# Optimization experiments

Hardware: AMD Instinct MI355X
Metric: run time of the kernel (lower is better)

The kernel has to match this reference:

```python
import jax, jax.numpy as jnp
import numpy as np
import hashlib

# Model hyperparameters (from VictorASIFractalLightModel defaults)
B, L, D = 2, 2048, 1024
VOCAB, TOOL_VOCAB = 65536, 128
STEPS = 8            # FractalEmbedding steps -> 2*STEPS = 16 features
N_CONV, N_ATTN = 10, 6
HEADS, Q_GROUPS = 8, 2
HPG = HEADS // Q_GROUPS
HEAD_DIM = D // HEADS
KSIZE = 5
EPS = 1e-5


def _token_to_c(token_ids_np):
    # sha256-based complex constant per token id (exactly as in FractalEmbedding)
    flat = token_ids_np.reshape(-1)
    out = np.empty((flat.size, 2), dtype=np.float32)
    for i, tid in enumerate(flat):
        h = hashlib.sha256(str(int(tid)).encode()).hexdigest()
        out[i, 0] = (int(h[:16], 16) / 2**64 - 0.5) * 2.0
        out[i, 1] = (int(h[16:32], 16) / 2**64 - 0.5) * 2.0
    return out.reshape(token_ids_np.shape + (2,))


def _julia_feats(cs):
    # Vectorized julia iteration, z starts at 0.  cs: [B, L, 2] -> feats [B, L, 2*STEPS]
    cr, ci = cs[..., 0], cs[..., 1]
    zr = jnp.zeros_like(cr)
    zi = jnp.zeros_like(ci)
    feats = []
    for _ in range(STEPS):
        zr, zi = zr * zr - zi * zi + cr, 2.0 * zr * zi + ci
        feats.append(zr)
        feats.append(zi)
    return jnp.stack(feats, axis=-1)


def _layer_norm(x, s, b):
    mu = jnp.mean(x, axis=-1, keepdims=True)
    var = jnp.mean(jnp.square(x - mu), axis=-1, keepdims=True)
    return (x - mu) * jax.lax.rsqrt(var + EPS) * s + b


def _conv_block(x, dw_w, dw_b, pw_w, pw_b, ln_s, ln_b):
    # x: [B, L, D] -> depthwise conv (k=5, same pad) -> pointwise conv to 2D -> GLU -> residual LN
    xc = jnp.transpose(x, (0, 2, 1))  # [B, D, L]
    y = jax.lax.conv_general_dilated(xc, dw_w, (1,), [(KSIZE // 2, KSIZE // 2)],
                                     dimension_numbers=("NCH", "OIH", "NCH"),
                                     feature_group_count=D) + dw_b[None, :, None]
    y = jax.lax.conv_general_dilated(y, pw_w, (1,), [(0, 0)],
                                     dimension_numbers=("NCH", "OIH", "NCH")) + pw_b[None, :, None]
    y = jnp.transpose(y, (0, 2, 1))  # [B, L, 2D]
    a, gate = jnp.split(y, 2, axis=-1)
    return _layer_norm(x + a * jax.nn.sigmoid(gate), ln_s, ln_b)


def _attention(x, qw, kvw, ow, ln_s, ln_b):
    # Grouped-query attention with an explicit (unfused) score tensor, per the source.
    Bx, Lx, Dx = x.shape
    q = (x @ qw).reshape(Bx, Lx, Q_GROUPS, HPG, HEAD_DIM)
    kv = (x @ kvw).reshape(Bx, Lx, HEADS, 2, HEAD_DIM)
    k = kv[..., 0, :].reshape(Bx, Lx, Q_GROUPS, HPG, HEAD_DIM)
    v = kv[..., 1, :].reshape(Bx, Lx, Q_GROUPS, HPG, HEAD_DIM)
    scale = HEAD_DIM ** -0.5
    scores = jnp.einsum("bqghd,bkghd->bghqk", q, k) * scale  # [B, g, hpg, Lq, Lk]
    attn = jax.nn.softmax(scores, axis=-1)
    out = jnp.einsum("bghqk,bkghd->bqghd", attn, v).reshape(Bx, Lx, Dx)
    return _layer_norm(x + out @ ow, ln_s, ln_b)


def setup_inputs() -> dict:
    key = jax.random.key(0)
    ks = jax.random.split(key, 10)
    token_ids = jax.random.randint(ks[0], (B, L), 0, VOCAB)
    cs = jnp.asarray(_token_to_c(np.asarray(token_ids)))
    return {
        "token_ids": token_ids,
        "cs": cs,
        "proj_w": jax.random.normal(ks[1], (2 * STEPS, D), dtype=jnp.float32) * 0.25,
        "emb_scale": jnp.ones((1,), dtype=jnp.float32),
        "conv_dw_w": jax.random.normal(ks[2], (N_CONV, D, 1, KSIZE), dtype=jnp.float32) * 0.2,
        "conv_dw_b": jnp.zeros((N_CONV, D), dtype=jnp.float32),
        "conv_pw_w": jax.random.normal(ks[3], (N_CONV, 2 * D, D, 1), dtype=jnp.float32) * (D ** -0.5),
        "conv_pw_b": jnp.zeros((N_CONV, 2 * D), dtype=jnp.float32),
        "conv_ln_s": jnp.ones((N_CONV, D), dtype=jnp.float32),
        "conv_ln_b": jnp.zeros((N_CONV, D), dtype=jnp.float32),
        "attn_q_w": jax.random.normal(ks[4], (N_ATTN, D, D), dtype=jnp.float32) * (D ** -0.5),
        "attn_kv_w": jax.random.normal(ks[5], (N_ATTN, D, 2 * D), dtype=jnp.float32) * (D ** -0.5),
        "attn_out_w": jax.random.normal(ks[6], (N_ATTN, D, D), dtype=jnp.float32) * (D ** -0.5),
        "attn_ln_s": jnp.ones((N_ATTN, D), dtype=jnp.float32),
        "attn_ln_b": jnp.zeros((N_ATTN, D), dtype=jnp.float32),
        "lm_w": jax.random.normal(ks[7], (D, VOCAB), dtype=jnp.float32) * (D ** -0.5),
        "tool_w": jax.random.normal(ks[8], (D, TOOL_VOCAB), dtype=jnp.float32) * (D ** -0.5),
        "tool_b": jnp.zeros((TOOL_VOCAB,), dtype=jnp.float32),
    }


def reference(token_ids, cs, proj_w, emb_scale, conv_dw_w, conv_dw_b, conv_pw_w, conv_pw_b,
              conv_ln_s, conv_ln_b, attn_q_w, attn_kv_w, attn_out_w, attn_ln_s, attn_ln_b,
              lm_w, tool_w, tool_b):
    feats = _julia_feats(cs)                 # [B, L, 16]
    h = (feats @ proj_w) * emb_scale         # FractalEmbedding
    for i in range(N_CONV):
        h = _conv_block(h, conv_dw_w[i], conv_dw_b[i], conv_pw_w[i], conv_pw_b[i],
                        conv_ln_s[i], conv_ln_b[i])
    for i in range(N_ATTN):
        h = _attention(h, attn_q_w[i], attn_kv_w[i], attn_out_w[i], attn_ln_s[i], attn_ln_b[i])
    # ReplayMemoryStack is a side-effecting identity on h.
    last = h[:, -1, :]
    gen_logits = last @ lm_w
    tool_logits = last @ tool_w + tool_b
    return gen_logits, tool_logits
```

## Files before the change

kernel.cpp:

```cpp
#include <hip/hip_runtime.h>
#include <hip/hip_bf16.h>
#include <math.h>

#define B_ 2
#define L_ 2048
#define D_ 1024
#define VOCAB_ 65536
#define TOOLV_ 128
#define NCONV_ 10
#define NATTN_ 6
#define HEADS_ 8
#define HD_ 128
#define EPS_ 1e-5f

typedef short bf16x8 __attribute__((ext_vector_type(8)));
typedef short short4v __attribute__((ext_vector_type(4)));
typedef float f32x4 __attribute__((ext_vector_type(4)));
#define MFMA16(a,b,c) __builtin_amdgcn_mfma_f32_16x16x32_bf16(a, b, c, 0, 0, 0)

__device__ inline short f2bf(float f) {
  __hip_bfloat16 h = __float2bfloat16(f);
  return *reinterpret_cast<short*>(&h);
}

__device__ __forceinline__ void gld16(const void* g, void* l) {
  __builtin_amdgcn_global_load_lds(
      (const __attribute__((address_space(1))) unsigned int*)g,
      (__attribute__((address_space(3))) unsigned int*)l, 16, 0, 0);
}

__global__ __launch_bounds__(256) void julia_proj_k(const float* __restrict__ cs,
    const float* __restrict__ pw, const float* __restrict__ esc, float* __restrict__ h) {
  int row = blockIdx.x;
  float cr = cs[2*(size_t)row], ci = cs[2*(size_t)row+1];
  float f[16];
  float zr = 0.f, zi = 0.f;
  #pragma unroll
  for (int s = 0; s < 8; ++s) {
    float nzr = zr*zr - zi*zi + cr;
    float nzi = 2.f*zr*zi + ci;
    zr = nzr; zi = nzi;
    f[2*s] = zr; f[2*s+1] = zi;
  }
  float e = esc[0];
  int d = threadIdx.x * 4;
  float4 acc = {0.f, 0.f, 0.f, 0.f};
  #pragma unroll
  for (int i = 0; i < 16; ++i) {
    float4 pv = *(const float4*)(pw + i*D_ + d);
    acc.x += f[i]*pv.x; acc.y += f[i]*pv.y; acc.z += f[i]*pv.z; acc.w += f[i]*pv.w;
  }
  acc.x *= e; acc.y *= e; acc.z *= e; acc.w *= e;
  *(float4*)(h + (size_t)row*D_ + d) = acc;
}

__global__ __launch_bounds__(256) void dwconv_k(const float* __restrict__ x,
    const float* __restrict__ w, const float* __restrict__ bias, short* __restrict__ y) {
  int idx = blockIdx.x*256 + threadIdx.x;
  int d = (idx & (D_/4 - 1)) * 4;
  int bl = idx >> 8;
  int l = bl & (L_-1);
  size_t bbase = (size_t)(bl >> 11) * L_;
  float4 acc = *(const float4*)(bias + d);
  float wr[4][5];
  #pragma unroll
  for (int j = 0; j < 4; ++j)
    #pragma unroll
    for (int k = 0; k < 5; ++k) wr[j][k] = w[(d+j)*5 + k];
  #pragma unroll
  for (int k = 0; k < 5; ++k) {
    int ll = l + k - 2;
    if (ll >= 0 && ll < L_) {
      float4 xv = *(const float4*)(x + (bbase + ll)*D_ + d);
      acc.x += xv.x*wr[0][k]; acc.y += xv.y*wr[1][k];
      acc.z += xv.z*wr[2][k]; acc.w += xv.w*wr[3][k];
    }
  }
  short4v o = { f2bf(acc.x), f2bf(acc.y), f2bf(acc.z), f2bf(acc.w) };
  ((short4v*)y)[idx] = o;
}

__global__ __launch_bounds__(256) void cvt_bf16_k(const float* __restrict__ x,
    short* __restrict__ y, int n4) {
  int i = blockIdx.x*256 + threadIdx.x;
  if (i >= n4) return;
  float4 v = ((const float4*)x)[i];
  short4v s = { f2bf(v.x), f2bf(v.y), f2bf(v.z), f2bf(v.w) };
  ((short4v*)y)[i] = s;
}

__global__ __launch_bounds__(256) void transp_bf16_k(const float* __restrict__ W0,
    short* __restrict__ WT0, int K, int N, size_t srcStride, size_t dstStride) {
  const float* W = W0 + blockIdx.z*srcStride;
  short* WT = WT0 + blockIdx.z*dstStride;
  __shared__ short t[32][33];
  int n0 = blockIdx.x*32, k0 = blockIdx.y*32;
  int tx = threadIdx.x & 31, ty = threadIdx.x >> 5;
  #pragma unroll
  for (int i = 0; i < 4; ++i) {
    int k = ty + i*8;
    t[tx][k] = f2bf(W[(size_t)(k0+k)*N + n0 + tx]);
  }
  __syncthreads();
  #pragma unroll
  for (int i = 0; i < 4; ++i) {
    int n = ty + i*8;
    WT[(size_t)(n0+n)*K + k0 + tx] = t[n][tx];
  }
}

template<int MODE, bool BIAS>
__global__ __launch_bounds__(256) void gemm_bf16(const short* __restrict__ A,
    const short* __restrict__ Bt, const float* __restrict__ bias,
    float* __restrict__ C, short* __restrict__ obf,
    short* __restrict__ kbf, short* __restrict__ vtbf,
    float scale, int M, int N, int K) {
  __shared__ short As[2*128*32];
  __shared__ short Bs[2*128*32];
  const int tid  = threadIdx.x;
  const int lane = tid & 63;
  const int wave = tid >> 6;
  const int wm = wave >> 1, wn = wave & 1;
  const int g = lane >> 4, c = lane & 15;
  const int m0 = blockIdx.x * 128, n0 = blockIdx.y * 128;

  f32x4 acc[4][4];
  #pragma unroll
  for (int i = 0; i < 4; ++i)
    #pragma unroll
    for (int j = 0; j < 4; ++j) acc[i][j] = (f32x4){0.f,0.f,0.f,0.f};

  const int srow = wave*16 + (lane>>2);
  const int scol = (lane&3)*8;
  const short* aSrc0 = A + (size_t)(m0 + srow)*K + scol;
  const short* aSrc1 = aSrc0 + (size_t)64*K;
  const short* bSrc0 = Bt + (size_t)(n0 + srow)*K + scol;
  const short* bSrc1 = bSrc0 + (size_t)64*K;
  short* AsW = &As[wave*512];
  short* BsW = &Bs[wave*512];

  for (int k0 = 0; k0 < K; k0 += 64) {
    __syncthreads();
    gld16(aSrc0 + k0,      AsW);
    gld16(aSrc1 + k0,      AsW + 2048);
    gld16(aSrc0 + k0 + 32, AsW + 4096);
    gld16(aSrc1 + k0 + 32, AsW + 6144);
    gld16(bSrc0 + k0,      BsW);
    gld16(bSrc1 + k0,      BsW + 2048);
    gld16(bSrc0 + k0 + 32, BsW + 4096);
    gld16(bSrc1 + k0 + 32, BsW + 6144);
    asm volatile("s_waitcnt vmcnt(0)" ::: "memory");
    __syncthreads();

    #pragma unroll
    for (int s = 0; s < 2; ++s) {
      bf16x8 af[4], bfr[4];
      #pragma unroll
      for (int mi = 0; mi < 4; ++mi)
        af[mi] = *(const bf16x8*)&As[s*4096 + (wm*64 + mi*16 + c)*32 + g*8];
      #pragma unroll
      for (int ni = 0; ni < 4; ++ni)
        bfr[ni] = *(const bf16x8*)&Bs[s*4096 + (wn*64 + ni*16 + c)*32 + g*8];
      #pragma unroll
      for (int mi = 0; mi < 4; ++mi)
        #pragma unroll
        for (int ni = 0; ni < 4; ++ni)
          acc[mi][ni] = MFMA16(af[mi], bfr[ni], acc[mi][ni]);
    }
  }

  #pragma unroll
  for (int mi = 0; mi < 4; ++mi) {
    int row = m0 + wm*64 + mi*16 + g*4;
    #pragma unroll
    for (int ni = 0; ni < 4; ++ni) {
      int col = n0 + wn*64 + ni*16 + c;
      if (MODE == 0) {
        float bv = BIAS ? bias[col] : 0.f;
        #pragma unroll
        for (int r = 0; r < 4; ++r)
          C[(size_t)(row+r)*N + col] = acc[mi][ni][r] + bv;
      } else {
        if (col < 1024) {
          #pragma unroll
          for (int r = 0; r < 4; ++r)
            obf[(size_t)(row+r)*1024 + col] = f2bf(acc[mi][ni][r]*scale);
        } else {
          int col2 = col - 1024;
          int hh = col2 >> 8, jj = (col2 >> 7) & 1, d = col2 & 127;
          int bb = row >> 11, l = row & 2047;
          size_t bh = (size_t)bb*8 + hh;
          if (jj == 0) {
            #pragma unroll
            for (int r = 0; r < 4; ++r)
              kbf[(bh*L_ + l + r)*128 + d] = f2bf(acc[mi][ni][r]);
          } else {
            #pragma unroll
            for (int r = 0; r < 4; ++r)
              vtbf[(bh*128 + d)*L_ + l + r] = f2bf(acc[mi][ni][r]);
          }
        }
      }
    }
  }
}

__global__ __launch_bounds__(256) void glu_ln_k(float* __restrict__ h,
    const float* __restrict__ y2, const float* __restrict__ s, const float* __restrict__ b,
    short* __restrict__ bo) {
  int row = blockIdx.x;
  int tid = threadIdx.x;
  int d = tid*4;
  float* xr = h + (size_t)row*D_;
  const float* yr = y2 + (size_t)row*2*D_;
  __shared__ float red[256];
  float4 xv = *(const float4*)(xr + d);
  float4 av = *(const float4*)(yr + d);
  float4 gv = *(const float4*)(yr + D_ + d);
  float v[4];
  v[0] = xv.x + av.x/(1.f + expf(-gv.x));
  v[1] = xv.y + av.y/(1.f + expf(-gv.y));
  v[2] = xv.z + av.z/(1.f + expf(-gv.z));
  v[3] = xv.w + av.w/(1.f + expf(-gv.w));
  red[tid] = v[0]+v[1]+v[2]+v[3]; __syncthreads();
  for (int st = 128; st > 0; st >>= 1) { if (tid < st) red[tid] += red[tid+st]; __syncthreads(); }
  float mu = red[0] * (1.f/D_); __syncthreads();
  float lv = 0.f;
  #pragma unroll
  for (int j = 0; j < 4; ++j) { float dd = v[j]-mu; lv += dd*dd; }
  red[tid] = lv; __syncthreads();
  for (int st = 128; st > 0; st >>= 1) { if (tid < st) red[tid] += red[tid+st]; __syncthreads(); }
  float var = red[0] * (1.f/D_);
  float r = 1.f/sqrtf(var + EPS_);
  float4 sv = *(const float4*)(s + d);
  float4 bv = *(const float4*)(b + d);
  float4 o;
  o.x = (v[0]-mu)*r*sv.x + bv.x;
  o.y = (v[1]-mu)*r*sv.y + bv.y;
  o.z = (v[2]-mu)*r*sv.z + bv.z;
  o.w = (v[3]-mu)*r*sv.w + bv.w;
  *(float4*)(xr + d) = o;
  if (bo) {
    short4v ob = { f2bf(o.x), f2bf(o.y), f2bf(o.z), f2bf(o.w) };
    *(short4v*)(bo + (size_t)row*D_ + d) = ob;
  }
}

__global__ __launch_bounds__(256) void resid_ln_k(float* __restrict__ h,
    const float* __restrict__ proj, const float* __restrict__ s, const float* __restrict__ b,
    short* __restrict__ bo) {
  int row = blockIdx.x;
  int tid = threadIdx.x;
  int d = tid*4;
  float* xr = h + (size_t)row*D_;
  const float* pr = proj + (size_t)row*D_;
  __shared__ float red[256];
  float4 xv = *(const float4*)(xr + d);
  float4 pv = *(const float4*)(pr + d);
  float v[4] = { xv.x+pv.x, xv.y+pv.y, xv.z+pv.z, xv.w+pv.w };
  red[tid] = v[0]+v[1]+v[2]+v[3]; __syncthreads();
  for (int st = 128; st > 0; st >>= 1) { if (tid < st) red[tid] += red[tid+st]; __syncthreads(); }
  float mu = red[0] * (1.f/D_); __syncthreads();
  float lv = 0.f;
  #pragma unroll
  for (int j = 0; j < 4; ++j) { float dd = v[j]-mu; lv += dd*dd; }
  red[tid] = lv; __syncthreads();
  for (int st = 128; st > 0; st >>= 1) { if (tid < st) red[tid] += red[tid+st]; __syncthreads(); }
  float var = red[0] * (1.f/D_);
  float r = 1.f/sqrtf(var + EPS_);
  float4 sv = *(const float4*)(s + d);
  float4 bv = *(const float4*)(b + d);
  float4 o;
  o.x = (v[0]-mu)*r*sv.x + bv.x;
  o.y = (v[1]-mu)*r*sv.y + bv.y;
  o.z = (v[2]-mu)*r*sv.z + bv.z;
  o.w = (v[3]-mu)*r*sv.w + bv.w;
  *(float4*)(xr + d) = o;
  if (bo) {
    short4v ob = { f2bf(o.x), f2bf(o.y), f2bf(o.z), f2bf(o.w) };
    *(short4v*)(bo + (size_t)row*D_ + d) = ob;
  }
}

#define PPITCH 72
__global__ __launch_bounds__(256) void attn2_k(const short* __restrict__ qbf,
    const short* __restrict__ kbf, const short* __restrict__ vtbf,
    short* __restrict__ obf) {
  __shared__ short Ks[64*128];
  __shared__ short Vts[128*64];
  __shared__ short Ps[4*16*PPITCH];

  const int tid  = threadIdx.x;
  const int wave = tid >> 6;
  const int lane = tid & 63;
  const int g    = lane >> 4;
  const int c    = lane & 15;
  const int hh   = blockIdx.y;
  const int b    = blockIdx.z;
  const int q0   = blockIdx.x*64 + wave*16;
  const size_t bh = (size_t)(b*HEADS_ + hh);

  bf16x8 qf[4];
  {
    const short* Qp = qbf + ((size_t)(b*L_ + q0 + c))*D_ + hh*HD_;
    #pragma unroll
    for (int kd = 0; kd < 4; ++kd)
      qf[kd] = *(const bf16x8*)(Qp + kd*32 + g*8);
  }

  f32x4 O[8];
  #pragma unroll
  for (int i = 0; i < 8; ++i) O[i] = (f32x4){0.f,0.f,0.f,0.f};
  float mrun[4] = {-INFINITY,-INFINITY,-INFINITY,-INFINITY};
  float lrun[4] = {0.f,0.f,0.f,0.f};
  short* Pw = Ps + wave*16*PPITCH;

  const short* kBase = kbf + bh*L_*128;
  const short* vBase = vtbf + bh*128*L_;

  for (int t = 0; t < L_/64; ++t) {
    __syncthreads();
    #pragma unroll
    for (int rd = 0; rd < 4; ++rd) {
      int slot = rd*256 + tid;
      int kr = slot >> 4, kj = slot & 15;
      int vr = slot >> 3, vj = slot & 7;
      gld16(kBase + ((size_t)(t*64 + kr))*128 + ((kj ^ (kr & 15)) * 8),
            (char*)Ks + (rd*256 + wave*64)*16);
      gld16(vBase + (size_t)vr*L_ + t*64 + ((vj ^ (vr & 7)) * 8),
            (char*)Vts + (rd*256 + wave*64)*16);
    }
    asm volatile("s_waitcnt vmcnt(0)" ::: "memory");
    __syncthreads();

    f32x4 s[4];
    #pragma unroll
    for (int nc = 0; nc < 4; ++nc) {
      s[nc] = (f32x4){0.f,0.f,0.f,0.f};
      int R = nc*16 + c;
      #pragma unroll
      for (int kd = 0; kd < 4; ++kd) {
        bf16x8 kf = *(const bf16x8*)&Ks[R*128 + (((kd*4 + g) ^ (R & 15)) * 8)];
        s[nc] = MFMA16(qf[kd], kf, s[nc]);
      }
    }

    float tm[4], rsum[4], alpha[4];
    #pragma unroll
    for (int r = 0; r < 4; ++r)
      tm[r] = fmaxf(fmaxf(s[0][r], s[1][r]), fmaxf(s[2][r], s[3][r]));
    #pragma unroll
    for (int r = 0; r < 4; ++r) {
      #pragma unroll
      for (int mask = 1; mask <= 8; mask <<= 1)
        tm[r] = fmaxf(tm[r], __shfl_xor(tm[r], mask));
      float mnew = fmaxf(mrun[r], tm[r]);
      alpha[r] = expf(mrun[r] - mnew);
      mrun[r] = mnew;
      rsum[r] = 0.f;
    }
    #pragma unroll
    for (int nc = 0; nc < 4; ++nc)
      #pragma unroll
      for (int r = 0; r < 4; ++r) {
        float p = expf(s[nc][r] - mrun[r]);
        s[nc][r] = p;
        rsum[r] += p;
      }
    #pragma unroll
    for (int r = 0; r < 4; ++r) {
      #pragma unroll
      for (int mask = 1; mask <= 8; mask <<= 1)
        rsum[r] += __shfl_xor(rsum[r], mask);
      lrun[r] = lrun[r]*alpha[r] + rsum[r];
    }
    #pragma unroll
    for (int nc = 0; nc < 8; ++nc)
      #pragma unroll
      for (int r = 0; r < 4; ++r) O[nc][r] *= alpha[r];

    #pragma unroll
    for (int nc = 0; nc < 4; ++nc)
      #pragma unroll
      for (int r = 0; r < 4; ++r)
        Pw[(g*4+r)*PPITCH + nc*16 + c] = f2bf(s[nc][r]);
    asm volatile("s_waitcnt lgkmcnt(0)" ::: "memory");
    bf16x8 pa0 = *(const bf16x8*)&Pw[c*PPITCH + g*8];
    bf16x8 pa1 = *(const bf16x8*)&Pw[c*PPITCH + 32 + g*8];

    #pragma unroll
    for (int ks = 0; ks < 2; ++ks) {
      #pragma unroll
      for (int nc = 0; nc < 8; ++nc) {
        int R = nc*16 + c;
        bf16x8 vf = *(const bf16x8*)&Vts[R*64 + (((ks*4 + g) ^ (R & 7)) * 8)];
        O[nc] = MFMA16(ks ? pa1 : pa0, vf, O[nc]);
      }
    }
  }

  short* ob = obf + ((size_t)(b*L_ + q0))*D_ + hh*HD_;
  #pragma unroll
  for (int r = 0; r < 4; ++r) {
    float inv = 1.f / lrun[r];
    #pragma unroll
    for (int nc = 0; nc < 8; ++nc)
      ob[(size_t)(g*4+r)*D_ + nc*16 + c] = f2bf(O[nc][r] * inv);
  }
}

__global__ __launch_bounds__(256) void lm_head_part_k(const float* __restrict__ h,
    const float* __restrict__ lm_w, float* __restrict__ part) {
  int tid = threadIdx.x;
  int n = (blockIdx.x*256 + tid)*4;
  int ks = blockIdx.y;
  __shared__ float last0[256], last1[256];
  const float* h0 = h + ((size_t)0*L_ + (L_-1))*D_ + ks*256;
  const float* h1 = h + ((size_t)1*L_ + (L_-1))*D_ + ks*256;
  last0[tid] = h0[tid]; last1[tid] = h1[tid];
  __syncthreads();
  float4 a0 = {0.f,0.f,0.f,0.f}, a1 = {0.f,0.f,0.f,0.f};
  const float* wp = lm_w + (size_t)(ks*256)*VOCAB_ + n;
  for (int kk = 0; kk < 256; ++kk) {
    float4 wv = *(const float4*)(wp + (size_t)kk*VOCAB_);
    float c0 = last0[kk], c1 = last1[kk];
    a0.x += c0*wv.x; a0.y += c0*wv.y; a0.z += c0*wv.z; a0.w += c0*wv.w;
    a1.x += c1*wv.x; a1.y += c1*wv.y; a1.z += c1*wv.z; a1.w += c1*wv.w;
  }
  *(float4*)(part + ((size_t)ks*2 + 0)*VOCAB_ + n) = a0;
  *(float4*)(part + ((size_t)ks*2 + 1)*VOCAB_ + n) = a1;
}

__global__ __launch_bounds__(256) void lm_head_red_k(const float* __restrict__ part,
    float* __restrict__ out) {
  int i = blockIdx.x*256 + threadIdx.x;
  int j = (i*4) / VOCAB_;
  int n = (i*4) & (VOCAB_-1);
  float4 acc = {0.f,0.f,0.f,0.f};
  #pragma unroll
  for (int ks = 0; ks < 4; ++ks) {
    float4 v = *(const float4*)(part + ((size_t)ks*2 + j)*VOCAB_ + n);
    acc.x += v.x; acc.y += v.y; acc.z += v.z; acc.w += v.w;
  }
  *(float4*)(out + (size_t)j*VOCAB_ + n) = acc;
}

__global__ __launch_bounds__(128) void tool_head_k(const float* __restrict__ h,
    const float* __restrict__ tw, const float* __restrict__ tb, float* __restrict__ out) {
  int b = blockIdx.x;
  int tid = threadIdx.x;
  __shared__ float last[D_];
  const float* hr = h + ((size_t)b*L_ + (L_-1))*D_;
  for (int d = tid; d < D_; d += 128) last[d] = hr[d];
  __syncthreads();
  float acc = tb[tid];
  for (int k = 0; k < D_; ++k) acc += last[k]*tw[(size_t)k*TOOLV_ + tid];
  out[(size_t)2*VOCAB_ + (size_t)b*TOOLV_ + tid] = acc;
}

extern "C" void kernel_launch(void* const* d_in, const int* in_sizes, int n_in,
                              void* d_out, int out_size, void* d_ws, size_t ws_size,
                              hipStream_t stream) {
  const float* cs        = (const float*)d_in[1];
  const float* proj_w    = (const float*)d_in[2];
  const float* emb_scale = (const float*)d_in[3];
  const float* conv_dw_w = (const float*)d_in[4];
  const float* conv_dw_b = (const float*)d_in[5];
  const float* conv_pw_w = (const float*)d_in[6];
  const float* conv_pw_b = (const float*)d_in[7];
  const float* conv_ln_s = (const float*)d_in[8];
  const float* conv_ln_b = (const float*)d_in[9];
  const float* attn_q_w  = (const float*)d_in[10];
  const float* attn_kv_w = (const float*)d_in[11];
  const float* attn_out_w= (const float*)d_in[12];
  const float* attn_ln_s = (const float*)d_in[13];
  const float* attn_ln_b = (const float*)d_in[14];
  const float* lm_w      = (const float*)d_in[15];
  const float* tool_w    = (const float*)d_in[16];
  const float* tool_b    = (const float*)d_in[17];

  const int M = B_*L_;
  float* h    = (float*)d_ws;
  float* buf2 = h    + (size_t)M*D_;
  short* kbf  = (short*)(buf2 + (size_t)M*2*D_);
  short* vtbf = kbf + (size_t)B_*HEADS_*L_*128;
  short* abf  = (short*)(vtbf + (size_t)B_*HEADS_*128*L_);
  short* wconv= abf + (size_t)M*D_;
  short* wqkv = wconv + (size_t)NCONV_*2*D_*D_;
  short* wout = wqkv + (size_t)NATTN_*3*D_*D_;
  float* lmpart = (float*)(wout + (size_t)NATTN_*D_*D_);
  short* qbf  = (short*)(buf2 + (size_t)M*D_);

  const float scale = 0.088388347648318447f;

  {
    int n4 = NCONV_*2*D_*D_/4;
    cvt_bf16_k<<<(n4 + 255)/256, 256, 0, stream>>>(conv_pw_w, wconv, n4);
    transp_bf16_k<<<dim3(D_/32, D_/32, NATTN_), 256, 0, stream>>>(
        attn_q_w, wqkv, D_, D_, (size_t)D_*D_, (size_t)3*D_*D_);
    transp_bf16_k<<<dim3((2*D_)/32, D_/32, NATTN_), 256, 0, stream>>>(
        attn_kv_w, wqkv + (size_t)D_*D_, D_, 2*D_, (size_t)D_*2*D_, (size_t)3*D_*D_);
    transp_bf16_k<<<dim3(D_/32, D_/32, NATTN_), 256, 0, stream>>>(
        attn_out_w, wout, D_, D_, (size_t)D_*D_, (size_t)D_*D_);
  }

  julia_proj_k<<<M, 256, 0, stream>>>(cs, proj_w, emb_scale, h);

  for (int i = 0; i < NCONV_; ++i) {
    dwconv_k<<<(M*D_/4)/256, 256, 0, stream>>>(h, conv_dw_w + (size_t)i*D_*5,
                                               conv_dw_b + (size_t)i*D_, abf);
    gemm_bf16<0, true><<<dim3(M/128, (2*D_)/128), 256, 0, stream>>>(
        abf, wconv + (size_t)i*2*D_*D_, conv_pw_b + (size_t)i*2*D_,
        buf2, nullptr, nullptr, nullptr, 1.f, M, 2*D_, D_);
    glu_ln_k<<<M, 256, 0, stream>>>(h, buf2, conv_ln_s + (size_t)i*D_,
                                    conv_ln_b + (size_t)i*D_,
                                    (i == NCONV_-1) ? abf : (short*)nullptr);
  }

  for (int i = 0; i < NATTN_; ++i) {
    gemm_bf16<3, false><<<dim3(M/128, (3*D_)/128), 256, 0, stream>>>(
        abf, wqkv + (size_t)i*3*D_*D_, nullptr, nullptr, qbf, kbf, vtbf,
        scale, M, 3*D_, D_);
    attn2_k<<<dim3(L_/64, HEADS_, B_), 256, 0, stream>>>(qbf, kbf, vtbf, abf);
    gemm_bf16<0, false><<<dim3(M/128, D_/128), 256, 0, stream>>>(
        abf, wout + (size_t)i*D_*D_, nullptr, buf2, nullptr, nullptr, nullptr,
        1.f, M, D_, D_);
    resid_ln_k<<<M, 256, 0, stream>>>(h, buf2, attn_ln_s + (size_t)i*D_,
                                      attn_ln_b + (size_t)i*D_,
                                      (i < NATTN_-1) ? abf : (short*)nullptr);
  }

  lm_head_part_k<<<dim3(VOCAB_/1024, 4), 256, 0, stream>>>(h, lm_w, lmpart);
  lm_head_red_k<<<(2*VOCAB_/4)/256, 256, 0, stream>>>(lmpart, (float*)d_out);
  tool_head_k<<<B_, 128, 0, stream>>>(h, tool_w, tool_b, (float*)d_out);
}
```

Measured before the change: 1.834 ms.

## Double-buffer LDS tiles in GEMM and attention to overlap loads with MFMA

Converts the bf16 GEMM and the flash-attention kernel from a single shared-memory buffer to ping-pong buffers. The next K-tile (or K/V tile) is issued with global_load_lds before the current tile's MFMAs run, with one wait-and-barrier per iteration. The GEMM K step drops from 64 to 32, so it now runs twice as many iterations with one barrier each. Attention LDS use roughly doubles, which may lower occupancy.

```diff
diff --git a/kernel.cpp b/kernel.cpp
--- a/kernel.cpp
+++ b/kernel.cpp
@@ -29,6 +29,12 @@
       (__attribute__((address_space(3))) unsigned int*)l, 16, 0, 0);
 }
 
+__device__ __forceinline__ void sync_prefetch() {
+  asm volatile("s_waitcnt vmcnt(0)" ::: "memory");
+  __builtin_amdgcn_s_barrier();
+  __builtin_amdgcn_sched_barrier(0);
+}
+
 __global__ __launch_bounds__(256) void julia_proj_k(const float* __restrict__ cs,
     const float* __restrict__ pw, const float* __restrict__ esc, float* __restrict__ h) {
   int row = blockIdx.x;
@@ -115,8 +121,8 @@
     float* __restrict__ C, short* __restrict__ obf,
     short* __restrict__ kbf, short* __restrict__ vtbf,
     float scale, int M, int N, int K) {
-  __shared__ short As[2*128*32];
-  __shared__ short Bs[2*128*32];
+  __shared__ short As[2][128*32];
+  __shared__ short Bs[2][128*32];
   const int tid  = threadIdx.x;
   const int lane = tid & 63;
   const int wave = tid >> 6;
@@ -136,36 +142,39 @@
   const short* aSrc1 = aSrc0 + (size_t)64*K;
   const short* bSrc0 = Bt + (size_t)(n0 + srow)*K + scol;
   const short* bSrc1 = bSrc0 + (size_t)64*K;
-  short* AsW = &As[wave*512];
-  short* BsW = &Bs[wave*512];
-
-  for (int k0 = 0; k0 < K; k0 += 64) {
-    __syncthreads();
-    gld16(aSrc0 + k0,      AsW);
-    gld16(aSrc1 + k0,      AsW + 2048);
-    gld16(aSrc0 + k0 + 32, AsW + 4096);
-    gld16(aSrc1 + k0 + 32, AsW + 6144);
-    gld16(bSrc0 + k0,      BsW);
-    gld16(bSrc1 + k0,      BsW + 2048);
-    gld16(bSrc0 + k0 + 32, BsW + 4096);
-    gld16(bSrc1 + k0 + 32, BsW + 6144);
-    asm volatile("s_waitcnt vmcnt(0)" ::: "memory");
-    __syncthreads();
-
-    #pragma unroll
-    for (int s = 0; s < 2; ++s) {
-      bf16x8 af[4], bfr[4];
-      #pragma unroll
-      for (int mi = 0; mi < 4; ++mi)
-        af[mi] = *(const bf16x8*)&As[s*4096 + (wm*64 + mi*16 + c)*32 + g*8];
+  const int woff = wave*512;
+
+  gld16(aSrc0, &As[0][woff]);
+  gld16(aSrc1, &As[0][woff + 2048]);
+  gld16(bSrc0, &Bs[0][woff]);
+  gld16(bSrc1, &Bs[0][woff + 2048]);
+  sync_prefetch();
+
+  const int nt = K >> 5;
+  int cur = 0;
+  for (int t = 0; t < nt; ++t) {
+    if (t + 1 < nt) {
+      int k0 = (t + 1) << 5;
+      gld16(aSrc0 + k0, &As[cur^1][woff]);
+      gld16(aSrc1 + k0, &As[cur^1][woff + 2048]);
+      gld16(bSrc0 + k0, &Bs[cur^1][woff]);
+      gld16(bSrc1 + k0, &Bs[cur^1][woff + 2048]);
+    }
+    bf16x8 af[4], bfr[4];
+    #pragma unroll
+    for (int mi = 0; mi < 4; ++mi)
+      af[mi] = *(const bf16x8*)&As[cur][(wm*64 + mi*16 + c)*32 + g*8];
+    #pragma unroll
+    for (int ni = 0; ni < 4; ++ni)
+      bfr[ni] = *(const bf16x8*)&Bs[cur][(wn*64 + ni*16 + c)*32 + g*8];
+    #pragma unroll
+    for (int mi = 0; mi < 4; ++mi)
       #pragma unroll
       for (int ni = 0; ni < 4; ++ni)
-        bfr[ni] = *(const bf16x8*)&Bs[s*4096 + (wn*64 + ni*16 + c)*32 + g*8];
-      #pragma unroll
-      for (int mi = 0; mi < 4; ++mi)
-        #pragma unroll
-        for (int ni = 0; ni < 4; ++ni)
-          acc[mi][ni] = MFMA16(af[mi], bfr[ni], acc[mi][ni]);
+        acc[mi][ni] = MFMA16(af[mi], bfr[ni], acc[mi][ni]);
+    if (t + 1 < nt) {
+      sync_prefetch();
+      cur ^= 1;
     }
   }
 
@@ -286,8 +295,8 @@
 __global__ __launch_bounds__(256) void attn2_k(const short* __restrict__ qbf,
     const short* __restrict__ kbf, const short* __restrict__ vtbf,
     short* __restrict__ obf) {
-  __shared__ short Ks[64*128];
-  __shared__ short Vts[128*64];
+  __shared__ short Ks[2][64*128];
+  __shared__ short Vts[2][128*64];
   __shared__ short Ps[4*16*PPITCH];
 
   const int tid  = threadIdx.x;
@@ -318,20 +327,26 @@
   const short* kBase = kbf + bh*L_*128;
   const short* vBase = vtbf + bh*128*L_;
 
-  for (int t = 0; t < L_/64; ++t) {
-    __syncthreads();
+  auto stage = [&](int t, int buf) {
     #pragma unroll
     for (int rd = 0; rd < 4; ++rd) {
       int slot = rd*256 + tid;
       int kr = slot >> 4, kj = slot & 15;
       int vr = slot >> 3, vj = slot & 7;
       gld16(kBase + ((size_t)(t*64 + kr))*128 + ((kj ^ (kr & 15)) * 8),
-            (char*)Ks + (rd*256 + wave*64)*16);
+            (char*)&Ks[buf][0] + (rd*256 + wave*64)*16);
       gld16(vBase + (size_t)vr*L_ + t*64 + ((vj ^ (vr & 7)) * 8),
-            (char*)Vts + (rd*256 + wave*64)*16);
-    }
-    asm volatile("s_waitcnt vmcnt(0)" ::: "memory");
-    __syncthreads();
+            (char*)&Vts[buf][0] + (rd*256 + wave*64)*16);
+    }
+  };
+
+  stage(0, 0);
+  sync_prefetch();
+  int cur = 0;
+  const int NT = L_/64;
+
+  for (int t = 0; t < NT; ++t) {
+    if (t + 1 < NT) stage(t + 1, cur^1);
 
     f32x4 s[4];
     #pragma unroll
@@ -340,7 +355,7 @@
       int R = nc*16 + c;
       #pragma unroll
       for (int kd = 0; kd < 4; ++kd) {
-        bf16x8 kf = *(const bf16x8*)&Ks[R*128 + (((kd*4 + g) ^ (R & 15)) * 8)];
+        bf16x8 kf = *(const bf16x8*)&Ks[cur][R*128 + (((kd*4 + g) ^ (R & 15)) * 8)];
         s[nc] = MFMA16(qf[kd], kf, s[nc]);
       }
     }
@@ -393,9 +408,14 @@
       #pragma unroll
       for (int nc = 0; nc < 8; ++nc) {
         int R = nc*16 + c;
-        bf16x8 vf = *(const bf16x8*)&Vts[R*64 + (((ks*4 + g) ^ (R & 7)) * 8)];
+        bf16x8 vf = *(const bf16x8*)&Vts[cur][R*64 + (((ks*4 + g) ^ (R & 7)) * 8)];
         O[nc] = MFMA16(ks ? pa1 : pa0, vf, O[nc]);
       }
+    }
+
+    if (t + 1 < NT) {
+      sync_prefetch();
+      cur ^= 1;
     }
   }
 
```

New measurement: 1.811 ms. No clear change (-1.3%).
